# Kernel tuning notes

Measured on AMD Instinct MI355X. Metric: run time of the kernel, lower is better.

## Reference

```python
import jax, jax.numpy as jnp
import numpy as np

B, C, J, T = 32, 128, 24, 128
Q, K = 6, 1024
EPS = 1e-10


def setup_inputs() -> dict:
    key = jax.random.key(0)
    k1, k2 = jax.random.split(key)
    x = jax.random.normal(k1, (B, C, J, T), dtype=jnp.float32)
    codebooks = jax.random.normal(k2, (Q, K, C), dtype=jnp.float32)
    return {"x": x, "codebooks": codebooks}


def reference(x, codebooks):
    """Residual VQ over 2D joint-temporal tokens.
    x: (B, C, J, T); codebooks: (Q, K, C).
    Returns (quantized_out (B,C,J,T), all_indices (B,J,T,Q), loss scalar, perplexity scalar).
    """
    b, c, j, t = x.shape
    q, k, _ = codebooks.shape
    # preprocess: (B, C, J, T) -> (B*J*T, C)
    xf = jnp.transpose(x, (0, 2, 3, 1)).reshape(-1, c)
    m = xf.shape[0]

    def step(carry, codebook):
        residual, q_out = carry
        # squared L2 distances (M, K)
        d = (jnp.sum(residual * residual, axis=-1, keepdims=True)
             - 2.0 * (residual @ codebook.T)
             + jnp.sum(codebook * codebook, axis=-1))
        idx = jnp.argmin(d, axis=-1)                       # (M,)
        xd = codebook[idx]                                 # dequantize (M, C)
        # commitment loss: mse(x, x_d.detach())
        loss = jnp.mean((residual - jax.lax.stop_gradient(xd)) ** 2)
        # perplexity from code usage histogram
        counts = jax.ops.segment_sum(jnp.ones((m,), xf.dtype), idx, num_segments=k)
        p = counts / m
        perp = jnp.exp(-jnp.sum(p * jnp.log(p + EPS)))
        # straight-through estimator
        quant = residual + jax.lax.stop_gradient(xd - residual)
        # residual = residual - quantized.detach(); quantized_out += quantized
        new_res = residual - jax.lax.stop_gradient(quant)
        return (new_res, q_out + quant), (idx, loss, perp)

    init = (xf, jnp.zeros_like(xf))
    (_, q_out), (idxs, losses, perps) = jax.lax.scan(step, init, codebooks)

    quantized_out = jnp.transpose(q_out.reshape(b, j, t, c), (0, 3, 1, 2))
    all_indices = jnp.transpose(idxs, (1, 0)).reshape(b, j, t, q)
    return quantized_out, all_indices, jnp.mean(losses), jnp.mean(perps)
```

## Files before the change

kernel.cpp:

```cpp
#include <hip/hip_runtime.h>

typedef __attribute__((ext_vector_type(8))) short short8v;
typedef __attribute__((ext_vector_type(4))) float f32x4;

#define B_ 32
#define C_ 128
#define J_ 24
#define T_ 128
#define Q_ 6
#define K_ 1024
#define JT (J_*T_)
#define M_ (B_*JT)
#define NBLK 768

#define OUT_QUANT 0
#define OUT_IDX   12582912
#define OUT_LOSS  13172736
#define OUT_PERP  13172737

#define TAU 0.02f

__device__ __forceinline__ unsigned short f2bf(float f) {
    unsigned int u = __float_as_uint(f);
    u = (u + 0x7FFFu + ((u >> 16) & 1u)) >> 16;
    return (unsigned short)u;
}
__device__ __forceinline__ float bf2f(unsigned short h) {
    return __uint_as_float(((unsigned int)h) << 16);
}

__device__ __forceinline__ void gload16(const void* g, void* lds) {
    __builtin_amdgcn_global_load_lds(
        (const __attribute__((address_space(1))) void*)g,
        (__attribute__((address_space(3))) void*)lds, 16, 0, 0);
}

__global__ __launch_bounds__(256) void c2_kernel(const float* __restrict__ cb,
                                                 float* __restrict__ c2) {
    int wave = (blockIdx.x * blockDim.x + threadIdx.x) >> 6;
    int lane = threadIdx.x & 63;
    if (wave >= Q_ * K_) return;
    const float2 v = reinterpret_cast<const float2*>(cb + (size_t)wave * C_)[lane];
    float s = v.x * v.x + v.y * v.y;
    #pragma unroll
    for (int off = 32; off; off >>= 1) s += __shfl_down(s, off, 64);
    if (lane == 0) c2[wave] = s;
}

__global__ __launch_bounds__(256) void cbtile_kernel(const float* __restrict__ cb,
                                                     unsigned short* __restrict__ cbt) {
    int i = blockIdx.x * 256 + threadIdx.x;
    if (i >= Q_ * 32 * 1024) return;
    int q = i >> 15;
    int rem = i & 32767;
    int tau = rem >> 10;
    int slot = rem & 1023;
    int part = slot >> 9;
    int ks = (slot >> 7) & 3;
    int nt = (slot >> 6) & 1;
    int r6 = slot & 63;
    int a = (r6 >> 4) & 3;
    int b3 = (r6 >> 3) & 1;
    int low3 = r6 & 7;
    int c4 = (b3 << 3) | (low3 ^ a);
    int code = tau * 32 + nt * 16 + c4;
    const float* src = cb + ((size_t)q * K_ + code) * C_ + ks * 32 + a * 8;
    short8v v;
    #pragma unroll
    for (int j = 0; j < 8; ++j) {
        float f = src[j];
        unsigned short hh = f2bf(f);
        v[j] = (part == 0) ? (short)hh : (short)f2bf(f - bf2f(hh));
    }
    *(short8v*)(cbt + (size_t)i * 8) = v;
}

__global__ __launch_bounds__(256) void transpose_kernel(const float* __restrict__ x,
                                                        float* __restrict__ res) {
    __shared__ float tile[32][33];
    const int tx = threadIdx.x & 31, ty = threadIdx.x >> 5;
    const int jt0 = blockIdx.x * 32;
    const int c0 = blockIdx.y * 32;
    const int b = blockIdx.z;
    const float* xb = x + ((size_t)b * C_ + c0) * JT + jt0;
    #pragma unroll
    for (int i = 0; i < 4; ++i) {
        int cc = ty + 8 * i;
        tile[cc][tx] = xb[(size_t)cc * JT + tx];
    }
    __syncthreads();
    float* rb = res + ((size_t)b * JT + jt0) * C_ + c0;
    #pragma unroll
    for (int i = 0; i < 4; ++i) {
        int jj = ty + 8 * i;
        rb[(size_t)jj * C_ + tx] = tile[tx][jj];
    }
}

__global__ __launch_bounds__(256, 2) void vq_fused_kernel(
        float* __restrict__ res,
        const float* __restrict__ cb,
        const unsigned short* __restrict__ cbt,
        const float* __restrict__ c2g,
        int* __restrict__ idxws, int* __restrict__ counts,
        float* __restrict__ partials) {
    __shared__ __attribute__((aligned(16))) unsigned short bs[4][8192];
    __shared__ float c2_lds[1024];
    __shared__ int idx_lds[128];
    __shared__ int nflag[4];
    __shared__ int flagl[4][32];
    __shared__ float wsum[4];
    __shared__ __attribute__((aligned(16))) float rowbuf[4][128];

    const int t = threadIdx.x;
    const int w = t >> 6, l = t & 63;
    const int la = l >> 4;
    const int lc = l & 15;
    const int rowbase = blockIdx.x * 128 + w * 32;
    const int lb = la * 256 + (l & 8) * 16 + (((l & 7) ^ la) * 16);

    float rres[64];
    #pragma unroll
    for (int mf = 0; mf < 2; ++mf) {
        const float* ap = res + (size_t)(rowbase + mf * 16 + lc) * C_ + la * 8;
        #pragma unroll
        for (int ks = 0; ks < 4; ++ks) {
            float4 f0 = *(const float4*)(ap + ks * 32);
            float4 f1 = *(const float4*)(ap + ks * 32 + 4);
            rres[mf * 32 + ks * 8 + 0] = f0.x; rres[mf * 32 + ks * 8 + 1] = f0.y;
            rres[mf * 32 + ks * 8 + 2] = f0.z; rres[mf * 32 + ks * 8 + 3] = f0.w;
            rres[mf * 32 + ks * 8 + 4] = f1.x; rres[mf * 32 + ks * 8 + 5] = f1.y;
            rres[mf * 32 + ks * 8 + 6] = f1.z; rres[mf * 32 + ks * 8 + 7] = f1.w;
        }
    }

#define STAGE(base_, tau_, slot_) { \
        const unsigned short* sp = (base_) + (size_t)(tau_) * 8192 + w * 2048 + l * 8; \
        char* dp = ((char*)bs[slot_]) + w * 4096; \
        gload16(sp, dp); \
        gload16(sp + 512, dp + 1024); \
        gload16(sp + 1024, dp + 2048); \
        gload16(sp + 1536, dp + 3072); \
    }

    for (int q = 0; q < Q_; ++q) {
        const int qk0 = q * K_;
        const unsigned short* cbase = cbt + (size_t)q * (32 * 8192);
        if (l == 0) nflag[w] = 0;

        float c2tmp[4];
        #pragma unroll
        for (int i = 0; i < 4; ++i) c2tmp[i] = c2g[qk0 + t + 256 * i];

        STAGE(cbase, 0, 0)
        STAGE(cbase, 1, 1)
        STAGE(cbase, 2, 2)

        #pragma unroll
        for (int i = 0; i < 4; ++i) c2_lds[t + 256 * i] = c2tmp[i];

        short8v ah[2][4], al[2][4];
        #pragma unroll
        for (int mf = 0; mf < 2; ++mf) {
            #pragma unroll
            for (int ks = 0; ks < 4; ++ks) {
                short8v vh, vl;
                #pragma unroll
                for (int j = 0; j < 8; ++j) {
                    float v = rres[mf * 32 + ks * 8 + j];
                    unsigned short hh = f2bf(v);
                    vh[j] = (short)hh;
                    vl[j] = (short)f2bf(v - bf2f(hh));
                }
                ah[mf][ks] = vh;
                al[mf][ks] = vl;
            }
        }

        float bd[2][4], bd2[2][4];
        int bi[2][4];
        #pragma unroll
        for (int mf = 0; mf < 2; ++mf)
            #pragma unroll
            for (int rg = 0; rg < 4; ++rg) {
                bd[mf][rg] = 3.4e38f; bd2[mf][rg] = 3.4e38f; bi[mf][rg] = 0;
            }

        asm volatile("s_waitcnt lgkmcnt(0)" ::: "memory");

        for (int tau = 0; tau < 32; ++tau) {
            if (tau < 30) {
                asm volatile("s_waitcnt vmcnt(8)" ::: "memory");
            } else if (tau == 30) {
                asm volatile("s_waitcnt vmcnt(4)" ::: "memory");
            } else {
                asm volatile("s_waitcnt vmcnt(0)" ::: "memory");
            }
            __builtin_amdgcn_s_barrier();
            if (tau < 29) STAGE(cbase, tau + 3, (tau + 3) & 3)

            const char* bufp = (const char*)bs[tau & 3];
            const float c2v0 = c2_lds[tau * 32 + lc];
            const float c2v1 = c2_lds[tau * 32 + 16 + lc];

            #pragma unroll
            for (int nt = 0; nt < 2; ++nt) {
                const int code = tau * 32 + nt * 16 + lc;
                const float c2v = nt ? c2v1 : c2v0;
                f32x4 aA0 = {0.f, 0.f, 0.f, 0.f}, aM0 = aA0, aA1 = aA0, aM1 = aA0;
                __builtin_amdgcn_s_setprio(1);
                #pragma unroll
                for (int ks = 0; ks < 4; ++ks) {
                    const char* bb = bufp + ks * 2048 + nt * 1024 + lb;
                    const short8v bh = *(const short8v*)(bb);
                    const short8v bl = *(const short8v*)(bb + 8192);
                    aA0 = __builtin_amdgcn_mfma_f32_16x16x32_bf16(ah[0][ks], bh, aA0, 0, 0, 0);
                    aM0 = __builtin_amdgcn_mfma_f32_16x16x32_bf16(al[0][ks], bh, aM0, 0, 0, 0);
                    aM0 = __builtin_amdgcn_mfma_f32_16x16x32_bf16(ah[0][ks], bl, aM0, 0, 0, 0);
                    aA1 = __builtin_amdgcn_mfma_f32_16x16x32_bf16(ah[1][ks], bh, aA1, 0, 0, 0);
                    aM1 = __builtin_amdgcn_mfma_f32_16x16x32_bf16(al[1][ks], bh, aM1, 0, 0, 0);
                    aM1 = __builtin_amdgcn_mfma_f32_16x16x32_bf16(ah[1][ks], bl, aM1, 0, 0, 0);
                }
                __builtin_amdgcn_s_setprio(0);
#define UPD(A, Mv, mf, rg) { \
                float s = A[rg] + Mv[rg]; \
                float d = fmaf(-2.f, s, c2v); \
                bool lt = d < bd[mf][rg]; \
                bd2[mf][rg] = lt ? bd[mf][rg] : fminf(bd2[mf][rg], d); \
                bd[mf][rg] = lt ? d : bd[mf][rg]; \
                bi[mf][rg] = lt ? code : bi[mf][rg]; }
                UPD(aA0, aM0, 0, 0) UPD(aA0, aM0, 0, 1) UPD(aA0, aM0, 0, 2) UPD(aA0, aM0, 0, 3)
                UPD(aA1, aM1, 1, 0) UPD(aA1, aM1, 1, 1) UPD(aA1, aM1, 1, 2) UPD(aA1, aM1, 1, 3)
#undef UPD
            }
        }

        #pragma unroll
        for (int mf = 0; mf < 2; ++mf) {
            #pragma unroll
            for (int rg = 0; rg < 4; ++rg) {
                float d1 = bd[mf][rg], d2 = bd2[mf][rg];
                int i1 = bi[mf][rg];
                #pragma unroll
                for (int off = 1; off < 16; off <<= 1) {
                    float od1 = __shfl_xor(d1, off);
                    float od2 = __shfl_xor(d2, off);
                    int oi1 = __shfl_xor(i1, off);
                    float nd2 = fminf(fminf(d2, od2), fmaxf(d1, od1));
                    if (od1 < d1 || (od1 == d1 && oi1 < i1)) { d1 = od1; i1 = oi1; }
                    d2 = nd2;
                }
                if (lc == 0) {
                    const int rr = mf * 16 + la * 4 + rg;
                    idx_lds[w * 32 + rr] = i1;
                    if (d2 - d1 < TAU) {
                        int p = atomicAdd(&nflag[w], 1);
                        flagl[w][p] = rr;
                    }
                }
            }
        }

        {
            const int nf = nflag[w];
            for (int f = 0; f < nf; ++f) {
                const int rr = flagl[w][f];
                const int mfr = rr >> 4, r16 = rr & 15;
                if (lc == r16) {
                    #pragma unroll
                    for (int ks = 0; ks < 4; ++ks) {
                        #pragma unroll
                        for (int j = 0; j < 8; ++j)
                            rowbuf[w][la * 8 + ks * 32 + j] =
                                (mfr == 0) ? rres[ks * 8 + j] : rres[32 + ks * 8 + j];
                    }
                }
                asm volatile("s_waitcnt lgkmcnt(0)" ::: "memory");
                __builtin_amdgcn_sched_barrier(0);
                const float4* rf4 = (const float4*)&rowbuf[w][0];
                double bdd = 1e300;
                int bk = 0;
                for (int kk = 0; kk < 16; ++kk) {
                    const int k = l + kk * 64;
                    const float4* bp4 = (const float4*)(cb + ((size_t)qk0 + k) * C_);
                    double s = 0.0;
                    for (int c4 = 0; c4 < 32; ++c4) {
                        float4 bv = bp4[c4];
                        float4 rv = rf4[c4];
                        double d0 = (double)rv.x - (double)bv.x; s = fma(d0, d0, s);
                        double d1 = (double)rv.y - (double)bv.y; s = fma(d1, d1, s);
                        double d2 = (double)rv.z - (double)bv.z; s = fma(d2, d2, s);
                        double d3 = (double)rv.w - (double)bv.w; s = fma(d3, d3, s);
                    }
                    if (s < bdd || (s == bdd && k < bk)) { bdd = s; bk = k; }
                }
                #pragma unroll
                for (int off = 1; off < 64; off <<= 1) {
                    double od = __shfl_xor(bdd, off);
                    int ok = __shfl_xor(bk, off);
                    if (od < bdd || (od == bdd && ok < bk)) { bdd = od; bk = ok; }
                }
                if (l == 0) idx_lds[w * 32 + rr] = bk;
                asm volatile("s_waitcnt lgkmcnt(0)" ::: "memory");
            }
        }

        if (l < 16) {
            const int k0 = idx_lds[w * 32 + l];
            const int k1 = idx_lds[w * 32 + 16 + l];
            idxws[(size_t)q * M_ + rowbase + l] = k0;
            idxws[(size_t)q * M_ + rowbase + 16 + l] = k1;
            atomicAdd(&counts[qk0 + k0], 1);
            atomicAdd(&counts[qk0 + k1], 1);
        }

        float sq = 0.f;
        #pragma unroll
        for (int mf = 0; mf < 2; ++mf) {
            const int k = idx_lds[w * 32 + mf * 16 + lc];
            const float* cbr = cb + ((size_t)qk0 + k) * C_ + la * 8;
            #pragma unroll
            for (int ks = 0; ks < 4; ++ks) {
                float4 cv0 = *(const float4*)(cbr + ks * 32);
                float4 cv1 = *(const float4*)(cbr + ks * 32 + 4);
                float cvv[8] = {cv0.x, cv0.y, cv0.z, cv0.w, cv1.x, cv1.y, cv1.z, cv1.w};
                #pragma unroll
                for (int j = 0; j < 8; ++j) {
                    float rv = rres[mf * 32 + ks * 8 + j];
                    float cvj = cvv[j];
                    float dd = rv - cvj;
                    sq += dd * dd;
                    rres[mf * 32 + ks * 8 + j] = rv - (rv + (cvj - rv));
                }
            }
        }
        #pragma unroll
        for (int off = 32; off; off >>= 1) sq += __shfl_down(sq, off, 64);
        if (l == 0) wsum[w] = sq;
        __syncthreads();
        if (t == 0) partials[q * NBLK + blockIdx.x] = wsum[0] + wsum[1] + wsum[2] + wsum[3];
        __syncthreads();
    }

    #pragma unroll
    for (int mf = 0; mf < 2; ++mf) {
        float* ap = res + (size_t)(rowbase + mf * 16 + lc) * C_ + la * 8;
        #pragma unroll
        for (int ks = 0; ks < 4; ++ks) {
            float4 f0 = *(const float4*)(ap + ks * 32);
            float4 f1 = *(const float4*)(ap + ks * 32 + 4);
            float4 o0, o1;
            o0.x = f0.x - rres[mf * 32 + ks * 8 + 0];
            o0.y = f0.y - rres[mf * 32 + ks * 8 + 1];
            o0.z = f0.z - rres[mf * 32 + ks * 8 + 2];
            o0.w = f0.w - rres[mf * 32 + ks * 8 + 3];
            o1.x = f1.x - rres[mf * 32 + ks * 8 + 4];
            o1.y = f1.y - rres[mf * 32 + ks * 8 + 5];
            o1.z = f1.z - rres[mf * 32 + ks * 8 + 6];
            o1.w = f1.w - rres[mf * 32 + ks * 8 + 7];
            *(float4*)(ap + ks * 32) = o0;
            *(float4*)(ap + ks * 32 + 4) = o1;
        }
    }
#undef STAGE
}

__global__ __launch_bounds__(256) void scalars_kernel(const float* __restrict__ partials,
                                                      const int* __restrict__ counts,
                                                      float* __restrict__ out) {
    __shared__ float red[256];
    const int t = threadIdx.x;
    float loss_acc = 0.f, perp_acc = 0.f;
    for (int q = 0; q < Q_; ++q) {
        float s = 0.f;
        for (int i = t; i < NBLK; i += 256) s += partials[q * NBLK + i];
        red[t] = s;
        __syncthreads();
        for (int o = 128; o; o >>= 1) {
            if (t < o) red[t] += red[t + o];
            __syncthreads();
        }
        if (t == 0) loss_acc += red[0] / (float)(M_ * C_);
        __syncthreads();
    }
    for (int q = 0; q < Q_; ++q) {
        float s = 0.f;
        for (int k = t; k < K_; k += 256) {
            float p = (float)counts[q * K_ + k] / (float)M_;
            s += p * logf(p + 1e-10f);
        }
        red[t] = s;
        __syncthreads();
        for (int o = 128; o; o >>= 1) {
            if (t < o) red[t] += red[t + o];
            __syncthreads();
        }
        if (t == 0) perp_acc += expf(-red[0]);
        __syncthreads();
    }
    if (t == 0) {
        out[OUT_LOSS] = loss_acc / (float)Q_;
        out[OUT_PERP] = perp_acc / (float)Q_;
    }
}

__global__ __launch_bounds__(256) void finalt_kernel(const float* __restrict__ qout,
                                                     float* __restrict__ out) {
    __shared__ float tile[32][33];
    const int tx = threadIdx.x & 31, ty = threadIdx.x >> 5;
    const int jt0 = blockIdx.x * 32;
    const int c0 = blockIdx.y * 32;
    const int b = blockIdx.z;
    const float* qb = qout + ((size_t)b * JT + jt0) * C_ + c0;
    #pragma unroll
    for (int i = 0; i < 4; ++i) {
        int jj = ty + 8 * i;
        tile[jj][tx] = qb[(size_t)jj * C_ + tx];
    }
    __syncthreads();
    float* ob = out + ((size_t)b * C_ + c0) * JT + jt0;
    #pragma unroll
    for (int i = 0; i < 4; ++i) {
        int cc = ty + 8 * i;
        ob[(size_t)cc * JT + tx] = tile[tx][cc];
    }
}

__global__ __launch_bounds__(256) void idxout_kernel(const int* __restrict__ idxin,
                                                     float* __restrict__ out) {
    int f = blockIdx.x * 256 + threadIdx.x;
    if (f >= M_ * Q_) return;
    int m = f / Q_;
    int q = f - m * Q_;
    out[f] = (float)idxin[q * M_ + m];
}

extern "C" void kernel_launch(void* const* d_in, const int* in_sizes, int n_in,
                              void* d_out, int out_size, void* d_ws, size_t ws_size,
                              hipStream_t stream) {
    const float* x = (const float*)d_in[0];
    const float* cb = (const float*)d_in[1];
    float* out = (float*)d_out;
    char* ws = (char*)d_ws;

    float* res = (float*)ws;
    int* idxws = (int*)(ws + 50331648);
    float* c2 = (float*)(ws + 52690944);
    int* counts = (int*)(ws + 52715520);
    float* partials = (float*)(ws + 52740096);
    unsigned short* cbt = (unsigned short*)(ws + 52758528);

    hipMemsetAsync(counts, 0, Q_ * K_ * sizeof(int), stream);
    c2_kernel<<<1536, 256, 0, stream>>>(cb, c2);
    cbtile_kernel<<<768, 256, 0, stream>>>(cb, cbt);
    transpose_kernel<<<dim3(96, 4, 32), 256, 0, stream>>>(x, res);
    vq_fused_kernel<<<NBLK, 256, 0, stream>>>(res, cb, cbt, c2, idxws, counts, partials);
    scalars_kernel<<<1, 256, 0, stream>>>(partials, counts, out);
    finalt_kernel<<<dim3(96, 4, 32), 256, 0, stream>>>(res, out);
    idxout_kernel<<<2304, 256, 0, stream>>>(idxws, out + OUT_IDX);
}
```

Baseline: 875.1 us.

## Restructure codebook pipeline to two tiles per barrier, lower fallback threshold

The main MFMA loop now handles two 32-code tiles per iteration, so there is one barrier and one wait per pair of tiles instead of one per tile. The squared codebook norms are read straight from global memory into registers one iteration ahead, replacing the shared-memory c2 table. The near-tie threshold that sends rows to the exact fp64 recheck drops from 0.02 to 0.008, so fewer rows take that slow path. The fp64 recheck also splits its sum across two accumulators to add instruction-level parallelism. The smaller threshold raises the risk that bf16-split rounding picks a different argmin than the reference, and the s_setprio hints are removed.

Result: faster. 767.6 us, median of 3 (-12.3%).

```diff
diff --git a/kernel.cpp b/kernel.cpp
--- a/kernel.cpp
+++ b/kernel.cpp
@@ -18,7 +18,7 @@
 #define OUT_LOSS  13172736
 #define OUT_PERP  13172737
 
-#define TAU 0.02f
+#define TAU 0.008f
 
 __device__ __forceinline__ unsigned short f2bf(float f) {
     unsigned int u = __float_as_uint(f);
@@ -105,7 +105,6 @@
         int* __restrict__ idxws, int* __restrict__ counts,
         float* __restrict__ partials) {
     __shared__ __attribute__((aligned(16))) unsigned short bs[4][8192];
-    __shared__ float c2_lds[1024];
     __shared__ int idx_lds[128];
     __shared__ int nflag[4];
     __shared__ int flagl[4][32];
@@ -134,9 +133,9 @@
         }
     }
 
-#define STAGE(base_, tau_, slot_) { \
+#define STAGE(base_, tau_) { \
         const unsigned short* sp = (base_) + (size_t)(tau_) * 8192 + w * 2048 + l * 8; \
-        char* dp = ((char*)bs[slot_]) + w * 4096; \
+        char* dp = ((char*)bs[(tau_) & 3]) + w * 4096; \
         gload16(sp, dp); \
         gload16(sp + 512, dp + 1024); \
         gload16(sp + 1024, dp + 2048); \
@@ -148,16 +147,14 @@
         const unsigned short* cbase = cbt + (size_t)q * (32 * 8192);
         if (l == 0) nflag[w] = 0;
 
-        float c2tmp[4];
-        #pragma unroll
-        for (int i = 0; i < 4; ++i) c2tmp[i] = c2g[qk0 + t + 256 * i];
-
-        STAGE(cbase, 0, 0)
-        STAGE(cbase, 1, 1)
-        STAGE(cbase, 2, 2)
-
-        #pragma unroll
-        for (int i = 0; i < 4; ++i) c2_lds[t + 256 * i] = c2tmp[i];
+        STAGE(cbase, 0)
+        STAGE(cbase, 1)
+        STAGE(cbase, 2)
+        STAGE(cbase, 3)
+        float c2v0 = c2g[qk0 + lc];
+        float c2v1 = c2g[qk0 + 16 + lc];
+        float c2v2 = c2g[qk0 + 32 + lc];
+        float c2v3 = c2g[qk0 + 48 + lc];
 
         short8v ah[2][4], al[2][4];
         #pragma unroll
@@ -186,52 +183,60 @@
                 bd[mf][rg] = 3.4e38f; bd2[mf][rg] = 3.4e38f; bi[mf][rg] = 0;
             }
 
-        asm volatile("s_waitcnt lgkmcnt(0)" ::: "memory");
-
-        for (int tau = 0; tau < 32; ++tau) {
-            if (tau < 30) {
-                asm volatile("s_waitcnt vmcnt(8)" ::: "memory");
-            } else if (tau == 30) {
+        asm volatile("s_waitcnt vmcnt(0)" ::: "memory");
+        __builtin_amdgcn_s_barrier();
+
+        for (int p = 0; p < 16; ++p) {
+            if (p < 15) {
+                STAGE(cbase, 2 * p + 2)
+                STAGE(cbase, 2 * p + 3)
+            }
+            float n0 = 0.f, n1 = 0.f, n2 = 0.f, n3 = 0.f;
+            if (p < 15) {
+                n0 = c2g[qk0 + (2 * p + 2) * 32 + lc];
+                n1 = c2g[qk0 + (2 * p + 2) * 32 + 16 + lc];
+                n2 = c2g[qk0 + (2 * p + 3) * 32 + lc];
+                n3 = c2g[qk0 + (2 * p + 3) * 32 + 16 + lc];
+            }
+
+            #pragma unroll
+            for (int tt = 0; tt < 2; ++tt) {
+                const int tau = 2 * p + tt;
+                const char* bufp = (const char*)bs[tau & 3];
+                #pragma unroll
+                for (int nt = 0; nt < 2; ++nt) {
+                    const int code = tau * 32 + nt * 16 + lc;
+                    const float c2v = tt ? (nt ? c2v3 : c2v2) : (nt ? c2v1 : c2v0);
+                    f32x4 aA0 = {0.f, 0.f, 0.f, 0.f}, aM0 = aA0, aA1 = aA0, aM1 = aA0;
+                    #pragma unroll
+                    for (int ks = 0; ks < 4; ++ks) {
+                        const char* bb = bufp + ks * 2048 + nt * 1024 + lb;
+                        const short8v bh = *(const short8v*)(bb);
+                        const short8v bl = *(const short8v*)(bb + 8192);
+                        aA0 = __builtin_amdgcn_mfma_f32_16x16x32_bf16(ah[0][ks], bh, aA0, 0, 0, 0);
+                        aM0 = __builtin_amdgcn_mfma_f32_16x16x32_bf16(al[0][ks], bh, aM0, 0, 0, 0);
+                        aM0 = __builtin_amdgcn_mfma_f32_16x16x32_bf16(ah[0][ks], bl, aM0, 0, 0, 0);
+                        aA1 = __builtin_amdgcn_mfma_f32_16x16x32_bf16(ah[1][ks], bh, aA1, 0, 0, 0);
+                        aM1 = __builtin_amdgcn_mfma_f32_16x16x32_bf16(al[1][ks], bh, aM1, 0, 0, 0);
+                        aM1 = __builtin_amdgcn_mfma_f32_16x16x32_bf16(ah[1][ks], bl, aM1, 0, 0, 0);
+                    }
+#define UPD(A, Mv, mf, rg) { \
+                    float s = A[rg] + Mv[rg]; \
+                    float d = fmaf(-2.f, s, c2v); \
+                    bool lt = d < bd[mf][rg]; \
+                    bd2[mf][rg] = lt ? bd[mf][rg] : fminf(bd2[mf][rg], d); \
+                    bd[mf][rg] = lt ? d : bd[mf][rg]; \
+                    bi[mf][rg] = lt ? code : bi[mf][rg]; }
+                    UPD(aA0, aM0, 0, 0) UPD(aA0, aM0, 0, 1) UPD(aA0, aM0, 0, 2) UPD(aA0, aM0, 0, 3)
+                    UPD(aA1, aM1, 1, 0) UPD(aA1, aM1, 1, 1) UPD(aA1, aM1, 1, 2) UPD(aA1, aM1, 1, 3)
+#undef UPD
+                }
+            }
+
+            if (p < 15) {
                 asm volatile("s_waitcnt vmcnt(4)" ::: "memory");
-            } else {
-                asm volatile("s_waitcnt vmcnt(0)" ::: "memory");
-            }
-            __builtin_amdgcn_s_barrier();
-            if (tau < 29) STAGE(cbase, tau + 3, (tau + 3) & 3)
-
-            const char* bufp = (const char*)bs[tau & 3];
-            const float c2v0 = c2_lds[tau * 32 + lc];
-            const float c2v1 = c2_lds[tau * 32 + 16 + lc];
-
-            #pragma unroll
-            for (int nt = 0; nt < 2; ++nt) {
-                const int code = tau * 32 + nt * 16 + lc;
-                const float c2v = nt ? c2v1 : c2v0;
-                f32x4 aA0 = {0.f, 0.f, 0.f, 0.f}, aM0 = aA0, aA1 = aA0, aM1 = aA0;
-                __builtin_amdgcn_s_setprio(1);
-                #pragma unroll
-                for (int ks = 0; ks < 4; ++ks) {
-                    const char* bb = bufp + ks * 2048 + nt * 1024 + lb;
-                    const short8v bh = *(const short8v*)(bb);
-                    const short8v bl = *(const short8v*)(bb + 8192);
-                    aA0 = __builtin_amdgcn_mfma_f32_16x16x32_bf16(ah[0][ks], bh, aA0, 0, 0, 0);
-                    aM0 = __builtin_amdgcn_mfma_f32_16x16x32_bf16(al[0][ks], bh, aM0, 0, 0, 0);
-                    aM0 = __builtin_amdgcn_mfma_f32_16x16x32_bf16(ah[0][ks], bl, aM0, 0, 0, 0);
-                    aA1 = __builtin_amdgcn_mfma_f32_16x16x32_bf16(ah[1][ks], bh, aA1, 0, 0, 0);
-                    aM1 = __builtin_amdgcn_mfma_f32_16x16x32_bf16(al[1][ks], bh, aM1, 0, 0, 0);
-                    aM1 = __builtin_amdgcn_mfma_f32_16x16x32_bf16(ah[1][ks], bl, aM1, 0, 0, 0);
-                }
-                __builtin_amdgcn_s_setprio(0);
-#define UPD(A, Mv, mf, rg) { \
-                float s = A[rg] + Mv[rg]; \
-                float d = fmaf(-2.f, s, c2v); \
-                bool lt = d < bd[mf][rg]; \
-                bd2[mf][rg] = lt ? bd[mf][rg] : fminf(bd2[mf][rg], d); \
-                bd[mf][rg] = lt ? d : bd[mf][rg]; \
-                bi[mf][rg] = lt ? code : bi[mf][rg]; }
-                UPD(aA0, aM0, 0, 0) UPD(aA0, aM0, 0, 1) UPD(aA0, aM0, 0, 2) UPD(aA0, aM0, 0, 3)
-                UPD(aA1, aM1, 1, 0) UPD(aA1, aM1, 1, 1) UPD(aA1, aM1, 1, 2) UPD(aA1, aM1, 1, 3)
-#undef UPD
+                __builtin_amdgcn_s_barrier();
+                c2v0 = n0; c2v1 = n1; c2v2 = n2; c2v3 = n3;
             }
         }
 
@@ -254,8 +259,8 @@
                     const int rr = mf * 16 + la * 4 + rg;
                     idx_lds[w * 32 + rr] = i1;
                     if (d2 - d1 < TAU) {
-                        int p = atomicAdd(&nflag[w], 1);
-                        flagl[w][p] = rr;
+                        int p2 = atomicAdd(&nflag[w], 1);
+                        flagl[w][p2] = rr;
                     }
                 }
             }
@@ -283,15 +288,20 @@
                 for (int kk = 0; kk < 16; ++kk) {
                     const int k = l + kk * 64;
                     const float4* bp4 = (const float4*)(cb + ((size_t)qk0 + k) * C_);
-                    double s = 0.0;
-                    for (int c4 = 0; c4 < 32; ++c4) {
-                        float4 bv = bp4[c4];
-                        float4 rv = rf4[c4];
-                        double d0 = (double)rv.x - (double)bv.x; s = fma(d0, d0, s);
-                        double d1 = (double)rv.y - (double)bv.y; s = fma(d1, d1, s);
-                        double d2 = (double)rv.z - (double)bv.z; s = fma(d2, d2, s);
-                        double d3 = (double)rv.w - (double)bv.w; s = fma(d3, d3, s);
+                    double s0 = 0.0, s1 = 0.0;
+                    for (int c4 = 0; c4 < 32; c4 += 2) {
+                        float4 bv0 = bp4[c4], bv1 = bp4[c4 + 1];
+                        float4 rv0 = rf4[c4], rv1 = rf4[c4 + 1];
+                        double e0 = (double)rv0.x - (double)bv0.x; s0 = fma(e0, e0, s0);
+                        double e1 = (double)rv0.y - (double)bv0.y; s0 = fma(e1, e1, s0);
+                        double e2 = (double)rv0.z - (double)bv0.z; s0 = fma(e2, e2, s0);
+                        double e3 = (double)rv0.w - (double)bv0.w; s0 = fma(e3, e3, s0);
+                        double f0 = (double)rv1.x - (double)bv1.x; s1 = fma(f0, f0, s1);
+                        double f1 = (double)rv1.y - (double)bv1.y; s1 = fma(f1, f1, s1);
+                        double f2 = (double)rv1.z - (double)bv1.z; s1 = fma(f2, f2, s1);
+                        double f3 = (double)rv1.w - (double)bv1.w; s1 = fma(f3, f3, s1);
                     }
+                    double s = s0 + s1;
                     if (s < bdd || (s == bdd && k < bk)) { bdd = s; bk = k; }
                 }
                 #pragma unroll
```
